# Kernel tuning notes

Hardware: AMD Instinct MI355X
Metric: run time of the kernel (lower is better)

Reference implementation:

```python
import jax, jax.numpy as jnp
import numpy as np

B, T, F, U = 128, 512, 512, 256

def hard_sigmoid(x):
    # Keras K.hard_sigmoid
    return jnp.clip(0.2 * x + 0.5, 0.0, 1.0)

def setup_inputs() -> dict:
    key = jax.random.key(0)
    ks = jax.random.split(key, 10)
    def glorot(k, shp):
        fan_in, fan_out = shp[0], shp[-1]
        std = np.sqrt(2.0 / (fan_in + fan_out)).astype(np.float32)
        return jax.random.normal(k, shp, jnp.float32) * std
    return {
        "x": jax.random.normal(ks[0], (B, T, F), jnp.float32),
        "kernel": glorot(ks[1], (F, 4 * U)),
        "recurrent_kernel": glorot(ks[2], (U, 4 * U)),
        "attention_h": glorot(ks[3], (F + U, U)),
        "attention_c": glorot(ks[4], (F + U, U)),
        "attention1": glorot(ks[5], (2 * U + F, U)),
        "biase1": glorot(ks[6], (U,)),
        "attention2": glorot(ks[7], (U, 1)),
        "attention2_2": glorot(ks[8], (U, 1)),
        "biase2": glorot(ks[9], (U,)),
    }

def _run_direction(x_tbf, xg_tbg, rk, Wh, Wc, units):
    # x_tbf: (T,B,F); xg_tbg: (T,B,4U) precomputed x @ kernel (same math as per-step dot)
    Bn = x_tbf.shape[1]
    z = jnp.zeros((Bn, units), x_tbf.dtype)
    carry0 = (z, z, z, z, z, z, z, z)

    def att_weights(states, Ws, xt):
        # softmax over L2 norms of tanh(concat(state, x) @ W) for 4 history states
        scores = []
        for s, W in zip(states, Ws):
            a = jnp.tanh(jnp.concatenate([s, xt], axis=1) @ W)  # (B,U)
            scores.append(jnp.sqrt(jnp.sum(a * a, axis=1)))     # (B,)
        return jax.nn.softmax(jnp.stack(scores, axis=1), axis=1)  # (B,4)

    def step(carry, inp):
        xt, xg = inp
        h1, c1, h2, c2, h3, c3, h4, c4 = carry
        wh = att_weights([h1, h2, h3, h4], [Wh, Wh, Wh, Wh], xt)
        hmix = jax.nn.relu(wh[:, 0:1] * h1 + wh[:, 1:2] * h2 + wh[:, 2:3] * h3 + wh[:, 3:4] * h4)
        # NOTE: original code (faithfully kept) uses attention_h for the 4th cell-state score
        wc = att_weights([c1, c2, c3, c4], [Wc, Wc, Wc, Wh], xt)
        cmix = jax.nn.relu(wc[:, 0:1] * c1 + wc[:, 1:2] * c2 + wc[:, 2:3] * c3 + wc[:, 3:4] * c4)
        g = xg + hmix @ rk  # (B,4U), gate order [i, f, c, o]
        i = hard_sigmoid(g[:, :units])
        f = hard_sigmoid(g[:, units:2 * units])
        m = hard_sigmoid(g[:, 2 * units:3 * units])  # candidate uses hard_sigmoid in original
        o = hard_sigmoid(g[:, 3 * units:])
        c = f * cmix + i * m
        h = o * jnp.tanh(c)
        # history shift: [h, c, h_tm1, c_tm1, h_tm2, c_tm2, h_tm3, c_tm3]
        return (h, c, h1, c1, h2, c2, h3, c3), h

    _, hs = jax.lax.scan(step, carry0, (x_tbf, xg_tbg))
    return hs  # (T,B,U)

def reference(x, kernel, recurrent_kernel, attention_h, attention_c,
              attention1, biase1, attention2, attention2_2, biase2):
    units = recurrent_kernel.shape[0]
    x_tbf = jnp.transpose(x, (1, 0, 2))              # (T,B,F)
    xg = jnp.einsum('tbf,fg->tbg', x_tbf, kernel)    # (T,B,4U)
    fwd = _run_direction(x_tbf, xg, recurrent_kernel, attention_h, attention_c, units)
    bwd = _run_direction(x_tbf[::-1], xg[::-1], recurrent_kernel, attention_h, attention_c, units)[::-1]
    outs = jnp.concatenate([fwd, bwd], axis=-1)      # (T,B,2U)
    outs = jnp.transpose(outs, (1, 0, 2))            # (B,T,2U)
    # intra attention (vectorized over time, equivalent to the per-step loop + reshape)
    A11 = attention1[:2 * units, :]
    A12 = attention1[2 * units:, :]
    ha = jax.nn.relu(outs @ A11 + 0.0 * biase1) @ attention2        # (B,T,1)
    hb = jax.nn.relu(x @ A12 + 0.0 * biase2) @ attention2_2         # (B,T,1)
    return jnp.tanh(ha * outs + hb)                                  # (B,T,2U)
```

## Files before the change

### kernel.cpp

```cpp
#include <hip/hip_runtime.h>
#include <cstddef>
#include <cstdint>

#define DEVINL __device__ __forceinline__

constexpr int Bn = 128;
constexpr int Tn = 512;
constexpr int Fn = 512;
constexpr int Un = 256;
constexpr int Gn = 1024;
constexpr int RS = 5;

typedef _Float16 h2t   __attribute__((ext_vector_type(2)));
typedef _Float16 half4 __attribute__((ext_vector_type(4)));
typedef _Float16 half8 __attribute__((ext_vector_type(8)));
typedef float    f32x4 __attribute__((ext_vector_type(4)));

DEVINL float ftanh(float x) { float e = __expf(2.f * x); return 1.f - 2.f / (e + 1.f); }
DEVINL float hsig(float x)  { return fminf(fmaxf(fmaf(x, 0.2f, 0.5f), 0.f), 1.f); }

DEVINL void softmax4(float* s) {
    float mx = fmaxf(fmaxf(s[0], s[1]), fmaxf(s[2], s[3]));
    float e0 = __expf(s[0] - mx), e1 = __expf(s[1] - mx);
    float e2 = __expf(s[2] - mx), e3 = __expf(s[3] - mx);
    float inv = 1.f / (e0 + e1 + e2 + e3);
    s[0] = e0 * inv; s[1] = e1 * inv; s[2] = e2 * inv; s[3] = e3 * inv;
}

DEVINL float d2(unsigned int w, unsigned int h, float acc) {
#if __has_builtin(__builtin_amdgcn_fdot2)
    return __builtin_amdgcn_fdot2(__builtin_bit_cast(h2t, w), __builtin_bit_cast(h2t, h), acc, false);
#else
    h2t a = __builtin_bit_cast(h2t, w), b = __builtin_bit_cast(h2t, h);
    acc = fmaf((float)a.x, (float)b.x, acc);
    acc = fmaf((float)a.y, (float)b.y, acc);
    return acc;
#endif
}
DEVINL float dot8h(uint4 w, uint4 h, float acc) {
    acc = d2(w.x, h.x, acc);
    acc = d2(w.y, h.y, acc);
    acc = d2(w.z, h.z, acc);
    acc = d2(w.w, h.w, acc);
    return acc;
}

__global__ __launch_bounds__(256)
void pack_x(const float* __restrict__ x, _Float16* __restrict__ xh)
{
    size_t i = ((size_t)blockIdx.x * 256 + threadIdx.x) * 4;
    float4 v = *(const float4*)(x + i);
    half4 o;
    o.x = (_Float16)v.x; o.y = (_Float16)v.y; o.z = (_Float16)v.z; o.w = (_Float16)v.w;
    *(half4*)(xh + i) = o;
}

__global__ __launch_bounds__(256)
void wt_pack(const float* __restrict__ W, _Float16* __restrict__ Wt, int N)
{
    int total = N * 512;
    for (int e = blockIdx.x * 256 + threadIdx.x; e < total; e += gridDim.x * 256) {
        int n = e >> 9, k = e & 511;
        Wt[e] = (_Float16)W[(size_t)k * N + n];
    }
}

__global__ __launch_bounds__(256)
void pack_w(const float* __restrict__ rk, const float* __restrict__ ath,
            const float* __restrict__ atc,
            _Float16* __restrict__ rkP, _Float16* __restrict__ WhP,
            _Float16* __restrict__ WcP)
{
    int idx = blockIdx.x * 256 + threadIdx.x;
    const int stride = gridDim.x * 256;
    for (int e = idx; e < 32 * 1024 * 8; e += stride) {
        int i = e & 7, n = (e >> 3) & 1023, kc = e >> 13;
        rkP[e] = (_Float16)rk[(size_t)(kc * 8 + i) * Gn + n];
    }
    for (int e = idx; e < 32 * 256 * 8; e += stride) {
        int i = e & 7, n = (e >> 3) & 255, kc = e >> 11;
        WhP[e] = (_Float16)ath[(size_t)(kc * 8 + i) * Un + n];
        WcP[e] = (_Float16)atc[(size_t)(kc * 8 + i) * Un + n];
    }
}

template<bool TMAJ>
__global__ __launch_bounds__(256)
void gemm_mfma(const _Float16* __restrict__ A, const _Float16* __restrict__ Wt,
               int N, _Float16* __restrict__ out)
{
    __shared__ __align__(16) _Float16 As[64][40];
    __shared__ __align__(16) _Float16 Bs[64][40];
    const int tid = threadIdx.x;
    const int n0 = blockIdx.x * 64, m0 = blockIdx.y * 64;
    const int w = tid >> 6, lane = tid & 63;
    const int fr = lane & 15, quad = lane >> 4;
    const int srow = tid >> 2, sk = (tid & 3) * 8;

    f32x4 acc[4];
    #pragma unroll
    for (int i = 0; i < 4; i++) acc[i] = (f32x4){0.f, 0.f, 0.f, 0.f};

    const _Float16* ap = A  + (size_t)(m0 + srow) * 512 + sk;
    const _Float16* bp = Wt + (size_t)(n0 + srow) * 512 + sk;

    for (int k0 = 0; k0 < 512; k0 += 32) {
        uint4 av = *(const uint4*)(ap + k0);
        uint4 bv = *(const uint4*)(bp + k0);
        __syncthreads();
        *(uint4*)&As[srow][sk] = av;
        *(uint4*)&Bs[srow][sk] = bv;
        __syncthreads();
        half8 a = *(const half8*)&As[w * 16 + fr][quad * 8];
        #pragma unroll
        for (int nt = 0; nt < 4; nt++) {
            half8 b = *(const half8*)&Bs[nt * 16 + fr][quad * 8];
            acc[nt] = __builtin_amdgcn_mfma_f32_16x16x32_f16(a, b, acc[nt], 0, 0, 0);
        }
    }
    #pragma unroll
    for (int nt = 0; nt < 4; nt++) {
        int n = n0 + nt * 16 + fr;
        #pragma unroll
        for (int reg = 0; reg < 4; reg++) {
            int m = m0 + w * 16 + quad * 4 + reg;
            if (TMAJ) {
                int b = m >> 9, t = m & 511;
                out[((size_t)t * Bn + b) * N + n] = (_Float16)acc[nt][reg];
            } else {
                out[(size_t)m * N + n] = (_Float16)acc[nt][reg];
            }
        }
    }
}

__global__ __launch_bounds__(512)
void recurrence(const _Float16* __restrict__ xg,
                const _Float16* __restrict__ xWh,
                const _Float16* __restrict__ xWc,
                const _Float16* __restrict__ rkP,
                const _Float16* __restrict__ WhP,
                const _Float16* __restrict__ WcP,
                _Float16* __restrict__ outs)
{
    const int tid = threadIdx.x;
    const int d = blockIdx.x >> 7;
    const int b = blockIdx.x & 127;

    __shared__ float Hr[RS][Un], Cr[RS][Un];
    __shared__ float PHr[RS][Un], PCcr[RS][Un], PChr[RS][Un];
    __shared__ __align__(16) unsigned int hm_pk[128];
    __shared__ __align__(16) unsigned int Hpk[128], Cpk[128];
    __shared__ float gtmp[4][Un];
    __shared__ __align__(16) float red[8][4];

    extern __shared__ __align__(16) uint4 WhL[];

    for (int e = tid; e < 8192; e += 512) WhL[e] = ((const uint4*)WhP)[e];
    for (int e = tid; e < RS * Un; e += 512) {
        ((float*)Hr)[e] = 0.f; ((float*)Cr)[e] = 0.f;
        ((float*)PHr)[e] = 0.f; ((float*)PCcr)[e] = 0.f; ((float*)PChr)[e] = 0.f;
    }
    __syncthreads();

    const int u = tid & 255;
    const int g = tid >> 8;
    const int lane = tid & 63;
    const int gwv = (tid >> 6) & 3;

    for (int t = 0; t < Tn; t++) {
        const int tt = d ? (Tn - 1 - t) : t;
        const int st = t % RS;
        int sj[4];
        #pragma unroll
        for (int j = 0; j < 4; j++) sj[j] = (t - 1 - j + 2 * RS) % RS;

        const size_t rowx = (size_t)tt * Bn + b;

        float xh = (float)xWh[rowx * Un + u];
        float xc = (float)xWc[rowx * Un + u];
        float xg0 = 0.f, xg1 = 0.f, xg2 = 0.f, xg3 = 0.f;
        if (tid < 256) {
            xg0 = (float)xg[rowx * Gn + u];
            xg1 = (float)xg[rowx * Gn + Un + u];
            xg2 = (float)xg[rowx * Gn + 2 * Un + u];
            xg3 = (float)xg[rowx * Gn + 3 * Un + u];
        }

        float vals[4];
        if (g == 0) {
            #pragma unroll
            for (int j = 0; j < 4; j++) {
                float ah = ftanh(PHr[sj[j]][u] + xh);
                vals[j] = ah * ah;
            }
        } else {
            #pragma unroll
            for (int j = 0; j < 4; j++) {
                float pc = (j < 3) ? PCcr[sj[j]][u] : PChr[sj[j]][u];
                float ac = ftanh(pc + ((j < 3) ? xc : xh));
                vals[j] = ac * ac;
            }
        }
        #pragma unroll
        for (int jj = 0; jj < 4; jj++) {
            float v = vals[jj];
            #pragma unroll
            for (int m = 32; m; m >>= 1) v += __shfl_xor(v, m, 64);
            if (lane == 0) red[g * 4 + jj][gwv] = v;
        }
        __syncthreads();

        float cmv = 0.f;
        if (tid < 256) {
            float sh[4], sc[4];
            #pragma unroll
            for (int j = 0; j < 4; j++) {
                float4 ph  = *(const float4*)red[j];
                float4 pcv = *(const float4*)red[4 + j];
                sh[j] = sqrtf(ph.x + ph.y + ph.z + ph.w);
                sc[j] = sqrtf(pcv.x + pcv.y + pcv.z + pcv.w);
            }
            softmax4(sh); softmax4(sc);
            float ha = 0.f, ca = 0.f;
            #pragma unroll
            for (int j = 0; j < 4; j++) {
                ha = fmaf(sh[j], Hr[sj[j]][u], ha);
                ca = fmaf(sc[j], Cr[sj[j]][u], ca);
            }
            float hmv = fmaxf(ha, 0.f);
            cmv = fmaxf(ca, 0.f);
            float ho = __shfl_xor(hmv, 1, 64);
            if (!(tid & 1)) {
                h2t pk; pk.x = (_Float16)hmv; pk.y = (_Float16)ho;
                hm_pk[u >> 1] = __builtin_bit_cast(unsigned int, pk);
            }
        }
        __syncthreads();

        {
            float a0 = 0.f, a1 = 0.f;
            const _Float16* p1 = rkP + (size_t)tid * 8;
            const _Float16* p2 = rkP + (size_t)(tid + 512) * 8;
            #pragma unroll 4
            for (int kc = 0; kc < 32; kc++) {
                uint4 w1 = *(const uint4*)(p1 + (size_t)kc * 8192);
                uint4 w2 = *(const uint4*)(p2 + (size_t)kc * 8192);
                uint4 h0 = *(const uint4*)&hm_pk[kc * 4];
                a0 = dot8h(w1, h0, a0);
                a1 = dot8h(w2, h0, a1);
            }
            int q = tid >> 8;
            gtmp[q][u] = a0;
            gtmp[q + 2][u] = a1;
        }
        __syncthreads();

        if (tid < 256) {
            float g0 = gtmp[0][u] + xg0;
            float g1 = gtmp[1][u] + xg1;
            float g2 = gtmp[2][u] + xg2;
            float g3 = gtmp[3][u] + xg3;
            float gi = hsig(g0), gf = hsig(g1), gm = hsig(g2), go = hsig(g3);
            float c = gf * cmv + gi * gm;
            float h = go * ftanh(c);
            Hr[st][u] = h;
            Cr[st][u] = c;
            outs[((size_t)b * Tn + tt) * 512 + d * 256 + u] = (_Float16)h;
            float hho = __shfl_xor(h, 1, 64);
            float cco = __shfl_xor(c, 1, 64);
            if (!(tid & 1)) {
                h2t pk1; pk1.x = (_Float16)h; pk1.y = (_Float16)hho;
                h2t pk2; pk2.x = (_Float16)c; pk2.y = (_Float16)cco;
                Hpk[u >> 1] = __builtin_bit_cast(unsigned int, pk1);
                Cpk[u >> 1] = __builtin_bit_cast(unsigned int, pk2);
            }
        }
        __syncthreads();

        if (tid < 256) {
            const int c = tid;
            float ph = 0.f, pch = 0.f;
            #pragma unroll 4
            for (int kc = 0; kc < 32; kc++) {
                uint4 wv4 = WhL[kc * 256 + c];
                uint4 Hv = *(const uint4*)&Hpk[kc * 4];
                uint4 Cv = *(const uint4*)&Cpk[kc * 4];
                ph  = dot8h(wv4, Hv, ph);
                pch = dot8h(wv4, Cv, pch);
            }
            PHr[st][c]  = ph;
            PChr[st][c] = pch;
        } else {
            const int c = tid - 256;
            const _Float16* pw = WcP + (size_t)c * 8;
            float pcc = 0.f;
            #pragma unroll 4
            for (int kc = 0; kc < 32; kc++) {
                uint4 wv4 = *(const uint4*)(pw + (size_t)kc * 2048);
                uint4 Cv = *(const uint4*)&Cpk[kc * 4];
                pcc = dot8h(wv4, Cv, pcc);
            }
            PCcr[st][c] = pcc;
        }
        __syncthreads();
    }
}

DEVINL void cvt8(uint4 v, float* f) {
    h2t p0 = __builtin_bit_cast(h2t, v.x), p1 = __builtin_bit_cast(h2t, v.y);
    h2t p2 = __builtin_bit_cast(h2t, v.z), p3 = __builtin_bit_cast(h2t, v.w);
    f[0] = (float)p0.x; f[1] = (float)p0.y; f[2] = (float)p1.x; f[3] = (float)p1.y;
    f[4] = (float)p2.x; f[5] = (float)p2.y; f[6] = (float)p3.x; f[7] = (float)p3.y;
}

__global__ __launch_bounds__(256)
void final2(const _Float16* __restrict__ t1, const _Float16* __restrict__ t2,
            const _Float16* __restrict__ outs16,
            const float* __restrict__ at2, const float* __restrict__ at22,
            float* __restrict__ out)
{
    __shared__ float has[8], hbs[8];
    const int tid = threadIdx.x;
    const size_t m0 = (size_t)blockIdx.x * 8;
    const int rr = tid >> 5, us = tid & 31;
    const size_t m = m0 + rr;

    uint4 v1 = *(const uint4*)(t1 + m * 256 + us * 8);
    uint4 v2 = *(const uint4*)(t2 + m * 256 + us * 8);
    float f1[8], f2[8];
    cvt8(v1, f1); cvt8(v2, f2);
    float4 wa0 = *(const float4*)(at2  + us * 8);
    float4 wa1 = *(const float4*)(at2  + us * 8 + 4);
    float4 wb0 = *(const float4*)(at22 + us * 8);
    float4 wb1 = *(const float4*)(at22 + us * 8 + 4);

    float pa = fmaxf(f1[0], 0.f) * wa0.x + fmaxf(f1[1], 0.f) * wa0.y
             + fmaxf(f1[2], 0.f) * wa0.z + fmaxf(f1[3], 0.f) * wa0.w
             + fmaxf(f1[4], 0.f) * wa1.x + fmaxf(f1[5], 0.f) * wa1.y
             + fmaxf(f1[6], 0.f) * wa1.z + fmaxf(f1[7], 0.f) * wa1.w;
    float pb = fmaxf(f2[0], 0.f) * wb0.x + fmaxf(f2[1], 0.f) * wb0.y
             + fmaxf(f2[2], 0.f) * wb0.z + fmaxf(f2[3], 0.f) * wb0.w
             + fmaxf(f2[4], 0.f) * wb1.x + fmaxf(f2[5], 0.f) * wb1.y
             + fmaxf(f2[6], 0.f) * wb1.z + fmaxf(f2[7], 0.f) * wb1.w;
    #pragma unroll
    for (int mm = 16; mm; mm >>= 1) {
        pa += __shfl_xor(pa, mm, 32);
        pb += __shfl_xor(pb, mm, 32);
    }
    if (us == 0) { has[rr] = pa; hbs[rr] = pb; }
    __syncthreads();

    for (int e = tid; e < 8 * 128; e += 256) {
        int r2 = e >> 7, k4 = (e & 127) * 4;
        size_t base = (m0 + r2) * 512 + k4;
        uint2 hv = *(const uint2*)(outs16 + base);
        h2t pA = __builtin_bit_cast(h2t, hv.x), pB = __builtin_bit_cast(h2t, hv.y);
        float hav = has[r2], hbv = hbs[r2];
        float4 o;
        o.x = ftanh(hav * (float)pA.x + hbv);
        o.y = ftanh(hav * (float)pA.y + hbv);
        o.z = ftanh(hav * (float)pB.x + hbv);
        o.w = ftanh(hav * (float)pB.y + hbv);
        *(float4*)(out + base) = o;
    }
}

extern "C" void kernel_launch(void* const* d_in, const int* in_sizes, int n_in,
                              void* d_out, int out_size, void* d_ws, size_t ws_size,
                              hipStream_t stream)
{
    (void)in_sizes; (void)n_in; (void)out_size; (void)ws_size;
    const float* x    = (const float*)d_in[0];
    const float* wk   = (const float*)d_in[1];
    const float* rk   = (const float*)d_in[2];
    const float* ath  = (const float*)d_in[3];
    const float* atc  = (const float*)d_in[4];
    const float* at1  = (const float*)d_in[5];
    const float* at2  = (const float*)d_in[7];
    const float* at22 = (const float*)d_in[8];
    float* out = (float*)d_out;

    char* p = (char*)d_ws;
    auto take = [&](size_t bytes) { char* q = p; p += (bytes + 255) & ~(size_t)255; return q; };
    _Float16* xg   = (_Float16*)take((size_t)Tn * Bn * Gn * 2);
    _Float16* xWh  = (_Float16*)take((size_t)Tn * Bn * Un * 2);
    _Float16* xWc  = (_Float16*)take((size_t)Tn * Bn * Un * 2);
    _Float16* A16  = (_Float16*)take((size_t)Bn * Tn * 512 * 2);
    _Float16* xf16 = (_Float16*)take((size_t)Bn * Tn * Fn * 2);
    _Float16* rkP  = (_Float16*)take((size_t)Un * Gn * 2);
    _Float16* WhP  = (_Float16*)take((size_t)Un * Un * 2);
    _Float16* WcP  = (_Float16*)take((size_t)Un * Un * 2);
    _Float16* Wt1  = (_Float16*)take((size_t)Gn * Fn * 2);
    _Float16* Wt2  = (_Float16*)take((size_t)Un * Fn * 2);
    _Float16* Wt3  = (_Float16*)take((size_t)Un * Fn * 2);
    _Float16* WtA  = (_Float16*)take((size_t)Un * Fn * 2);
    _Float16* WtB  = (_Float16*)take((size_t)Un * Fn * 2);
    _Float16* t1 = (_Float16*)xg;
    _Float16* t2 = t1 + (size_t)Bn * Tn * Un;

    pack_x<<<32768, 256, 0, stream>>>(x, xf16);
    wt_pack<<<2048, 256, 0, stream>>>(wk, Wt1, Gn);
    wt_pack<<<1024, 256, 0, stream>>>(ath + (size_t)Un * Un, Wt2, Un);
    wt_pack<<<1024, 256, 0, stream>>>(atc + (size_t)Un * Un, Wt3, Un);
    wt_pack<<<1024, 256, 0, stream>>>(at1, WtA, Un);
    wt_pack<<<1024, 256, 0, stream>>>(at1 + (size_t)512 * Un, WtB, Un);
    pack_w<<<64, 256, 0, stream>>>(rk, ath, atc, rkP, WhP, WcP);

    gemm_mfma<true><<<dim3(Gn / 64, (Bn * Tn) / 64), 256, 0, stream>>>(xf16, Wt1, Gn, xg);
    gemm_mfma<true><<<dim3(Un / 64, (Bn * Tn) / 64), 256, 0, stream>>>(xf16, Wt2, Un, xWh);
    gemm_mfma<true><<<dim3(Un / 64, (Bn * Tn) / 64), 256, 0, stream>>>(xf16, Wt3, Un, xWc);

    hipFuncSetAttribute(reinterpret_cast<const void*>(recurrence),
                        hipFuncAttributeMaxDynamicSharedMemorySize, 131072);
    recurrence<<<dim3(256), dim3(512), 131072, stream>>>(xg, xWh, xWc, rkP, WhP, WcP, A16);

    gemm_mfma<false><<<dim3(Un / 64, (Bn * Tn) / 64), 256, 0, stream>>>(A16,  WtA, Un, t1);
    gemm_mfma<false><<<dim3(Un / 64, (Bn * Tn) / 64), 256, 0, stream>>>(xf16, WtB, Un, t2);
    final2<<<(Bn * Tn) / 8, 256, 0, stream>>>(t1, t2, A16, at2, at22, out);
}
```

Before: 4.771 ms.

## Double recurrence block to 1024 threads to split per-step work

```diff
diff --git a/kernel.cpp b/kernel.cpp
--- a/kernel.cpp
+++ b/kernel.cpp
@@ -134,7 +134,7 @@
     }
 }
 
-__global__ __launch_bounds__(512)
+__global__ __launch_bounds__(1024)
 void recurrence(const _Float16* __restrict__ xg,
                 const _Float16* __restrict__ xWh,
                 const _Float16* __restrict__ xWc,
@@ -156,17 +156,18 @@
 
     extern __shared__ __align__(16) uint4 WhL[];
 
-    for (int e = tid; e < 8192; e += 512) WhL[e] = ((const uint4*)WhP)[e];
-    for (int e = tid; e < RS * Un; e += 512) {
+    for (int e = tid; e < 8192; e += 1024) WhL[e] = ((const uint4*)WhP)[e];
+    for (int e = tid; e < RS * Un; e += 1024) {
         ((float*)Hr)[e] = 0.f; ((float*)Cr)[e] = 0.f;
         ((float*)PHr)[e] = 0.f; ((float*)PCcr)[e] = 0.f; ((float*)PChr)[e] = 0.f;
     }
     __syncthreads();
 
-    const int u = tid & 255;
-    const int g = tid >> 8;
+    const int u    = tid & 255;
+    const int fam  = tid >> 9;
+    const int jj2  = (tid >> 8) & 1;
     const int lane = tid & 63;
-    const int gwv = (tid >> 6) & 3;
+    const int gwv  = (tid >> 6) & 3;
 
     for (int t = 0; t < Tn; t++) {
         const int tt = d ? (Tn - 1 - t) : t;
@@ -178,36 +179,35 @@
         const size_t rowx = (size_t)tt * Bn + b;
 
         float xh = (float)xWh[rowx * Un + u];
-        float xc = (float)xWc[rowx * Un + u];
+        float xc = (fam == 1) ? (float)xWc[rowx * Un + u] : 0.f;
         float xg0 = 0.f, xg1 = 0.f, xg2 = 0.f, xg3 = 0.f;
         if (tid < 256) {
+            xc  = (float)xWc[rowx * Un + u];
             xg0 = (float)xg[rowx * Gn + u];
             xg1 = (float)xg[rowx * Gn + Un + u];
             xg2 = (float)xg[rowx * Gn + 2 * Un + u];
             xg3 = (float)xg[rowx * Gn + 3 * Un + u];
         }
 
-        float vals[4];
-        if (g == 0) {
-            #pragma unroll
-            for (int j = 0; j < 4; j++) {
-                float ah = ftanh(PHr[sj[j]][u] + xh);
-                vals[j] = ah * ah;
-            }
-        } else {
-            #pragma unroll
-            for (int j = 0; j < 4; j++) {
+        float vals[2];
+        #pragma unroll
+        for (int jj = 0; jj < 2; jj++) {
+            int j = jj2 * 2 + jj;
+            float a;
+            if (fam == 0) {
+                a = ftanh(PHr[sj[j]][u] + xh);
+            } else {
                 float pc = (j < 3) ? PCcr[sj[j]][u] : PChr[sj[j]][u];
-                float ac = ftanh(pc + ((j < 3) ? xc : xh));
-                vals[j] = ac * ac;
-            }
+                a = ftanh(pc + ((j < 3) ? xc : xh));
+            }
+            vals[jj] = a * a;
         }
         #pragma unroll
-        for (int jj = 0; jj < 4; jj++) {
+        for (int jj = 0; jj < 2; jj++) {
             float v = vals[jj];
             #pragma unroll
             for (int m = 32; m; m >>= 1) v += __shfl_xor(v, m, 64);
-            if (lane == 0) red[g * 4 + jj][gwv] = v;
+            if (lane == 0) red[fam * 4 + jj2 * 2 + jj][gwv] = v;
         }
         __syncthreads();
 
@@ -239,20 +239,15 @@
         __syncthreads();
 
         {
-            float a0 = 0.f, a1 = 0.f;
+            float a0 = 0.f;
             const _Float16* p1 = rkP + (size_t)tid * 8;
-            const _Float16* p2 = rkP + (size_t)(tid + 512) * 8;
             #pragma unroll 4
             for (int kc = 0; kc < 32; kc++) {
                 uint4 w1 = *(const uint4*)(p1 + (size_t)kc * 8192);
-                uint4 w2 = *(const uint4*)(p2 + (size_t)kc * 8192);
                 uint4 h0 = *(const uint4*)&hm_pk[kc * 4];
                 a0 = dot8h(w1, h0, a0);
-                a1 = dot8h(w2, h0, a1);
-            }
-            int q = tid >> 8;
-            gtmp[q][u] = a0;
-            gtmp[q + 2][u] = a1;
+            }
+            gtmp[tid >> 8][u] = a0;
         }
         __syncthreads();
 
@@ -291,7 +286,7 @@
             }
             PHr[st][c]  = ph;
             PChr[st][c] = pch;
-        } else {
+        } else if (tid < 512) {
             const int c = tid - 256;
             const _Float16* pw = WcP + (size_t)c * 8;
             float pcc = 0.f;
@@ -413,7 +408,7 @@
 
     hipFuncSetAttribute(reinterpret_cast<const void*>(recurrence),
                         hipFuncAttributeMaxDynamicSharedMemorySize, 131072);
-    recurrence<<<dim3(256), dim3(512), 131072, stream>>>(xg, xWh, xWc, rkP, WhP, WcP, A16);
+    recurrence<<<dim3(256), dim3(1024), 131072, stream>>>(xg, xWh, xWc, rkP, WhP, WcP, A16);
 
     gemm_mfma<false><<<dim3(Un / 64, (Bn * Tn) / 64), 256, 0, stream>>>(A16,  WtA, Un, t1);
     gemm_mfma<false><<<dim3(Un / 64, (Bn * Tn) / 64), 256, 0, stream>>>(xf16, WtB, Un, t2);
```

Measured after the change: 4.651 ms. 1.03x faster.
